# Kernel optimization log

Measured on AMD Instinct MI355X. Metric: run time of the kernel, lower is better.

## Reference

```python
import jax, jax.numpy as jnp
import numpy as np

# dims
B, SP, SF = 8, 1024, 1024
XD, YD = 6, 1
D, L, H, W = 512, 4, 8, 128
DH = D // H
S = SP + SF           # 2048 total sequence
C = S // W            # 16 clusters
FF = 4 * D
MIN_STD = 0.01


def _ln(x, g, b):
    m = x.mean(-1, keepdims=True)
    v = ((x - m) ** 2).mean(-1, keepdims=True)
    return (x - m) * jax.lax.rsqrt(v + 1e-5) * g + b


def _routing_attn(x, Wq, Wk, Wv, Wo, means):
    # x: (B,S,D); means: (H,C,DH) k-means centroids for routing
    b, s, _ = x.shape
    proj = lambda Wm: (x @ Wm).reshape(b, s, H, DH).transpose(0, 2, 1, 3)  # bhsd
    q, k, v = proj(Wq), proj(Wk), proj(Wv)
    qn = q * jax.lax.rsqrt((q * q).sum(-1, keepdims=True) + 1e-8)
    kn = k * jax.lax.rsqrt((k * k).sum(-1, keepdims=True) + 1e-8)
    # route: each cluster grabs its top-W most similar tokens (queries and keys separately)
    iq = jax.lax.top_k(jnp.einsum('bhsd,hcd->bhcs', qn, means), W)[1].reshape(b, H, C * W)
    ik = jax.lax.top_k(jnp.einsum('bhsd,hcd->bhcs', kn, means), W)[1].reshape(b, H, C * W)
    gather = lambda t, i: jnp.take_along_axis(t, i[..., None], axis=2).reshape(b, H, C, W, DH)
    qg, kg, vg = gather(q, iq), gather(k, ik), gather(v, ik)
    dots = jnp.einsum('bhcid,bhcjd->bhcij', qg, kg) * (DH ** -0.5)  # within-cluster attention
    attn = jax.nn.softmax(dots, axis=-1)
    og = jnp.einsum('bhcij,bhcjd->bhcid', attn, vg).reshape(b, H, C * W, DH)
    # scatter-mean back to sequence positions (a token may be routed to several clusters)
    bi = jnp.arange(b)[:, None, None]
    hi = jnp.arange(H)[None, :, None]
    out = jnp.zeros((b, H, s, DH), x.dtype).at[bi, hi, iq].add(og)
    cnt = jnp.zeros((b, H, s, 1), x.dtype).at[bi, hi, iq].add(1.0)
    out = out / jnp.maximum(cnt, 1.0)
    out = out.transpose(0, 2, 1, 3).reshape(b, s, D)
    return out @ Wo


def setup_inputs() -> dict:
    key = jax.random.key(0)
    ks = jax.random.split(key, 16)
    n = lambda k, shp, sc=0.02: (jax.random.normal(k, shp) * sc).astype(jnp.float32)
    inp = {
        'past_x': n(ks[0], (B, SP, XD), 1.0),
        'past_y': n(ks[1], (B, SP, YD), 1.0),
        'future_x': n(ks[2], (B, SF, XD), 1.0),
        'W_emb': n(ks[3], (XD + YD, D)), 'b_emb': jnp.zeros((D,), jnp.float32),
        'ln1_g': jnp.ones((L, D), jnp.float32), 'ln1_b': jnp.zeros((L, D), jnp.float32),
        'Wq': n(ks[4], (L, D, D)), 'Wk': n(ks[5], (L, D, D)),
        'Wv': n(ks[6], (L, D, D)), 'Wo': n(ks[7], (L, D, D)),
        'means': n(ks[8], (L, H, C, DH), 1.0),
        'ln2_g': jnp.ones((L, D), jnp.float32), 'ln2_b': jnp.zeros((L, D), jnp.float32),
        'W1': n(ks[9], (L, D, FF)), 'b1': jnp.zeros((L, FF), jnp.float32),
        'W2': n(ks[10], (L, FF, D)), 'b2': jnp.zeros((L, D), jnp.float32),
        'lnf_g': jnp.ones((D,), jnp.float32), 'lnf_b': jnp.zeros((D,), jnp.float32),
        'W_mean': n(ks[11], (D, YD)), 'b_mean': jnp.zeros((YD,), jnp.float32),
        'W_std': n(ks[12], (D, YD)), 'b_std': jnp.zeros((YD,), jnp.float32),
    }
    return inp


def reference(past_x, past_y, future_x, W_emb, b_emb, ln1_g, ln1_b, Wq, Wk, Wv, Wo,
              means, ln2_g, ln2_b, W1, b1, W2, b2, lnf_g, lnf_b, W_mean, b_mean,
              W_std, b_std):
    # future targets faked by repeating last observed y (as in the torch module)
    future_y_fake = jnp.repeat(past_y[:, -1:, :], SF, axis=1)
    context = jnp.concatenate([past_x, past_y], -1)
    target = jnp.concatenate([future_x, future_y_fake], -1)
    x = jnp.concatenate([context, target], 1)          # (B, S, XD+YD)
    h = x @ W_emb + b_emb                              # enc_emb
    for l in range(L):                                 # routing-transformer encoder
        h = h + _routing_attn(_ln(h, ln1_g[l], ln1_b[l]), Wq[l], Wk[l], Wv[l], Wo[l], means[l])
        hn = _ln(h, ln2_g[l], ln2_b[l])
        h = h + (jax.nn.gelu(hn @ W1[l] + b1[l]) @ W2[l] + b2[l])
    h = _ln(h, lnf_g, lnf_b)
    mean = (h @ W_mean + b_mean)[:, SP:, :]
    log_sigma = (h @ W_std + b_std)[:, SP:, :]
    sigma = MIN_STD + (1.0 - MIN_STD) * jax.nn.softplus(log_sigma)
    return mean, sigma
```

## Files before the change

kernel.cpp:

```cpp
#include <hip/hip_runtime.h>
#include <hip/hip_bf16.h>

constexpr int Bc  = 8;
constexpr int SPc = 1024;
constexpr int SFc = 1024;
constexpr int Sc  = 2048;
constexpr int Dc  = 512;
constexpr int Lc  = 4;
constexpr int Hc  = 8;
constexpr int Wc  = 128;
constexpr int DHc = 64;
constexpr int Cc  = 16;
constexpr int FFc = 2048;
constexpr int Mrows = Bc * Sc;

__global__ __launch_bounds__(256) void embed_kernel(
    const float* __restrict__ px, const float* __restrict__ py,
    const float* __restrict__ fx, const float* __restrict__ We,
    const float* __restrict__ be, float* __restrict__ h)
{
  int i = blockIdx.x * 256 + threadIdx.x;
  int d  = i & 511;
  int bs = i >> 9;
  int s  = bs & (Sc - 1);
  int b  = bs >> 11;
  float x[7];
  if (s < SPc) {
    int r = b * SPc + s;
#pragma unroll
    for (int t = 0; t < 6; ++t) x[t] = px[r * 6 + t];
    x[6] = py[r];
  } else {
    int r = b * SFc + (s - SPc);
#pragma unroll
    for (int t = 0; t < 6; ++t) x[t] = fx[r * 6 + t];
    x[6] = py[b * SPc + SPc - 1];
  }
  double a = (double)be[d];
#pragma unroll
  for (int t = 0; t < 7; ++t) a = fma((double)x[t], (double)We[t * Dc + d], a);
  h[i] = (float)a;
}

__global__ __launch_bounds__(256) void ln_kernel(
    const float* __restrict__ x, const float* __restrict__ g,
    const float* __restrict__ bb, float* __restrict__ o)
{
  int row = blockIdx.x;
  const float* xr = x + (size_t)row * Dc;
  float* orow = o + (size_t)row * Dc;
  int tid = threadIdx.x;
  float v0 = xr[tid], v1 = xr[tid + 256];
  double s = (double)v0 + (double)v1;
  double sq = (double)v0 * v0 + (double)v1 * v1;
  __shared__ double ra[4], rb[4];
  int lane = tid & 63, w = tid >> 6;
#pragma unroll
  for (int off = 32; off; off >>= 1) { s += __shfl_down(s, off); sq += __shfl_down(sq, off); }
  if (lane == 0) { ra[w] = s; rb[w] = sq; }
  __syncthreads();
  s  = ra[0] + ra[1] + ra[2] + ra[3];
  sq = rb[0] + rb[1] + rb[2] + rb[3];
  double m   = s * (1.0 / Dc);
  double var = sq * (1.0 / Dc) - m * m;
  double rs  = 1.0 / sqrt(var + 1e-5);
  orow[tid]       = (float)(((double)v0 - m) * rs * (double)g[tid]       + (double)bb[tid]);
  orow[tid + 256] = (float)(((double)v1 - m) * rs * (double)g[tid + 256] + (double)bb[tid + 256]);
}

__device__ __forceinline__ float gelu_tanh(float v) {
  float x3 = v * v * v;
  return 0.5f * v * (1.0f + tanhf(0.7978845608028654f * (v + 0.044715f * x3)));
}

template<bool BIAS, bool GELU_, bool RES>
__global__ __launch_bounds__(256) void gemm128(
    const float* __restrict__ A, const float* __restrict__ Bm,
    const float* __restrict__ bias, float* __restrict__ Cm,
    int N, int K)
{
  constexpr int BM = 128, BN = 128, BK = 16;
  __shared__ float As[BK][BM + 4];
  __shared__ float Bs[BK][BN + 4];
  const int tid = threadIdx.x;
  const int tx = tid & 15, ty = tid >> 4;
  const int nbn = N >> 7;
  const int bm = blockIdx.x / nbn, bn = blockIdx.x % nbn;
  const float* Ab = A + (size_t)bm * BM * K;
  const float* Bb = Bm + bn * BN;
  double acc[8][8] = {};

  for (int k0 = 0; k0 < K; k0 += BK) {
#pragma unroll
    for (int r = 0; r < 8; ++r) {
      int e = r * 256 + tid;
      int m = e >> 4, kk = e & 15;
      As[kk][m] = Ab[(size_t)m * K + k0 + kk];
    }
#pragma unroll
    for (int r = 0; r < 8; ++r) {
      int e = r * 256 + tid;
      int kk = e >> 7, n = e & 127;
      Bs[kk][n] = Bb[(size_t)(k0 + kk) * N + n];
    }
    __syncthreads();
#pragma unroll
    for (int kk = 0; kk < BK; ++kk) {
      float a[8], bf[8];
      *(float4*)&a[0]  = *(const float4*)&As[kk][ty * 8];
      *(float4*)&a[4]  = *(const float4*)&As[kk][ty * 8 + 4];
      *(float4*)&bf[0] = *(const float4*)&Bs[kk][tx * 8];
      *(float4*)&bf[4] = *(const float4*)&Bs[kk][tx * 8 + 4];
#pragma unroll
      for (int i = 0; i < 8; ++i)
#pragma unroll
        for (int j = 0; j < 8; ++j)
          acc[i][j] = fma((double)a[i], (double)bf[j], acc[i][j]);
    }
    __syncthreads();
  }
#pragma unroll
  for (int i = 0; i < 8; ++i) {
    int row = bm * BM + ty * 8 + i;
    float* crow = Cm + (size_t)row * N + bn * BN;
#pragma unroll
    for (int j = 0; j < 8; ++j) {
      double vd = acc[i][j];
      int col = tx * 8 + j;
      if (BIAS)  vd += (double)bias[bn * BN + col];
      float v = (float)vd;
      if (GELU_) v = gelu_tanh(v);
      if (RES)   v += crow[col];
      crow[col] = v;
    }
  }
}

__global__ __launch_bounds__(256) void scores_kernel(
    const float* __restrict__ q, const float* __restrict__ means,
    float* __restrict__ sc)
{
  int gw   = blockIdx.x * 4 + (threadIdx.x >> 6);
  int lane = threadIdx.x & 63;
  int h  = gw & 7;
  int bs = gw >> 3;
  int s  = bs & (Sc - 1);
  int b  = bs >> 11;
  float qv = q[(size_t)bs * Dc + h * DHc + lane];
  double sq = (double)qv * (double)qv;
#pragma unroll
  for (int off = 32; off; off >>= 1) sq += __shfl_xor(sq, off);
  double qn = (double)qv / sqrt(sq + 1e-8);
  double myval = 0.0;
#pragma unroll
  for (int c = 0; c < Cc; ++c) {
    double p = qn * (double)means[(h * Cc + c) * DHc + lane];
#pragma unroll
    for (int off = 32; off; off >>= 1) p += __shfl_xor(p, off);
    if (lane == c) myval = p;
  }
  if (lane < Cc)
    sc[(((size_t)b * Hc + h) * Cc + lane) * Sc + s] = (float)myval;
}

__global__ __launch_bounds__(256) void topk_kernel(
    const float* __restrict__ sc, int* __restrict__ idx_out)
{
  __shared__ float sv[Sc];
  __shared__ int   si[Sc];
  int base = blockIdx.x * Sc;
  int tid = threadIdx.x;
  for (int i = tid; i < Sc; i += 256) { sv[i] = sc[base + i]; si[i] = i; }
  __syncthreads();
  for (int k = 2; k <= Sc; k <<= 1) {
    for (int j = k >> 1; j > 0; j >>= 1) {
      for (int i = tid; i < Sc; i += 256) {
        int ixj = i ^ j;
        if (ixj > i) {
          bool asc = (i & k) != 0;
          float a = sv[i], b2 = sv[ixj];
          if (asc ? (a > b2) : (a < b2)) {
            sv[i] = b2; sv[ixj] = a;
            int t = si[i]; si[i] = si[ixj]; si[ixj] = t;
          }
        }
      }
      __syncthreads();
    }
  }
  if (tid < Wc) idx_out[blockIdx.x * Wc + tid] = si[tid];
}

__global__ __launch_bounds__(128) void attn_kernel(
    const float* __restrict__ q, const float* __restrict__ k,
    const float* __restrict__ v, const int* __restrict__ iq,
    const int* __restrict__ ik, float* __restrict__ accum,
    float* __restrict__ cnt)
{
  __shared__ float ks[Wc][DHc];
  __shared__ float vs[Wc][DHc];
  __shared__ int iqs[Wc], iks[Wc];
  int blk = blockIdx.x;
  int tid = threadIdx.x;
  int bh = blk / Cc;
  int h = bh & 7, b = bh >> 3;
  iqs[tid] = iq[blk * Wc + tid];
  iks[tid] = ik[blk * Wc + tid];
  __syncthreads();
  for (int e = tid; e < Wc * DHc; e += 128) {
    int j = e >> 6, d = e & 63;
    size_t off = ((size_t)b * Sc + iks[j]) * Dc + h * DHc + d;
    ks[j][d] = k[off];
    vs[j][d] = v[off];
  }
  __syncthreads();

  size_t qoff = ((size_t)b * Sc + iqs[tid]) * Dc + h * DHc;
  float qr[DHc];
  const float4* q4 = (const float4*)(q + qoff);
#pragma unroll
  for (int d4 = 0; d4 < 16; ++d4) {
    float4 t = q4[d4];
    qr[4 * d4] = t.x; qr[4 * d4 + 1] = t.y; qr[4 * d4 + 2] = t.z; qr[4 * d4 + 3] = t.w;
  }
  double m = -1e300, lsum = 0.0;
  double acc[DHc];
#pragma unroll
  for (int d = 0; d < DHc; ++d) acc[d] = 0.0;

  for (int j = 0; j < Wc; ++j) {
    const float* krow = ks[j];
    double s = 0.0;
#pragma unroll
    for (int d = 0; d < DHc; ++d)
      s = fma((double)qr[d], (double)krow[d], s);
    s *= 0.125;
    double mn = fmax(m, s);
    double scale = exp(m - mn);
    double p = exp(s - mn);
    lsum = lsum * scale + p;
    const float* vrow = vs[j];
#pragma unroll
    for (int d = 0; d < DHc; ++d)
      acc[d] = fma(acc[d], scale, p * (double)vrow[d]);
    m = mn;
  }
  double inv = 1.0 / lsum;
  float* arow = accum + qoff;
#pragma unroll
  for (int d = 0; d < DHc; ++d) atomicAdd(&arow[d], (float)(acc[d] * inv));
  atomicAdd(&cnt[((size_t)b * Sc + iqs[tid]) * Hc + h], 1.0f);
}

__global__ __launch_bounds__(256) void div_kernel(
    float* __restrict__ accum, const float* __restrict__ cnt)
{
  size_t i = (size_t)blockIdx.x * 256 + threadIdx.x;
  float c = cnt[i >> 6];
  accum[i] /= fmaxf(c, 1.0f);
}

__global__ __launch_bounds__(256) void final_kernel(
    const float* __restrict__ h, const float* __restrict__ g,
    const float* __restrict__ be, const float* __restrict__ wm,
    const float* __restrict__ bm, const float* __restrict__ wsd,
    const float* __restrict__ bsd, float* __restrict__ out)
{
  int blk = blockIdx.x;
  int b = blk >> 10, sf = blk & 1023;
  const float* hr = h + ((size_t)b * Sc + SPc + sf) * Dc;
  int tid = threadIdx.x;
  float v0 = hr[tid], v1 = hr[tid + 256];
  double s = (double)v0 + (double)v1;
  double sq = (double)v0 * v0 + (double)v1 * v1;
  __shared__ double ra[4], rb[4];
  int lane = tid & 63, w = tid >> 6;
#pragma unroll
  for (int off = 32; off; off >>= 1) { s += __shfl_down(s, off); sq += __shfl_down(sq, off); }
  if (lane == 0) { ra[w] = s; rb[w] = sq; }
  __syncthreads();
  s  = ra[0] + ra[1] + ra[2] + ra[3];
  sq = rb[0] + rb[1] + rb[2] + rb[3];
  double m   = s * (1.0 / Dc);
  double var = sq * (1.0 / Dc) - m * m;
  double rs  = 1.0 / sqrt(var + 1e-5);
  double n0 = ((double)v0 - m) * rs * (double)g[tid]       + (double)be[tid];
  double n1 = ((double)v1 - m) * rs * (double)g[tid + 256] + (double)be[tid + 256];
  double d1 = n0 * (double)wm[tid]  + n1 * (double)wm[tid + 256];
  double d2 = n0 * (double)wsd[tid] + n1 * (double)wsd[tid + 256];
  __syncthreads();
#pragma unroll
  for (int off = 32; off; off >>= 1) { d1 += __shfl_down(d1, off); d2 += __shfl_down(d2, off); }
  if (lane == 0) { ra[w] = d1; rb[w] = d2; }
  __syncthreads();
  if (tid == 0) {
    double mean = ra[0] + ra[1] + ra[2] + ra[3] + (double)bm[0];
    double ls   = rb[0] + rb[1] + rb[2] + rb[3] + (double)bsd[0];
    double sp = fmax(ls, 0.0) + log1p(exp(-fabs(ls)));
    out[blk] = (float)mean;
    out[Bc * SFc + blk] = (float)(0.01 + 0.99 * sp);
  }
}

extern "C" void kernel_launch(void* const* d_in, const int* in_sizes, int n_in,
                              void* d_out, int out_size, void* d_ws, size_t ws_size,
                              hipStream_t stream) {
  (void)in_sizes; (void)n_in; (void)out_size; (void)ws_size;
  const float* past_x   = (const float*)d_in[0];
  const float* past_y   = (const float*)d_in[1];
  const float* future_x = (const float*)d_in[2];
  const float* W_emb    = (const float*)d_in[3];
  const float* b_emb    = (const float*)d_in[4];
  const float* ln1_g    = (const float*)d_in[5];
  const float* ln1_b    = (const float*)d_in[6];
  const float* Wq       = (const float*)d_in[7];
  const float* Wk       = (const float*)d_in[8];
  const float* Wv       = (const float*)d_in[9];
  const float* Wo       = (const float*)d_in[10];
  const float* means    = (const float*)d_in[11];
  const float* ln2_g    = (const float*)d_in[12];
  const float* ln2_b    = (const float*)d_in[13];
  const float* W1       = (const float*)d_in[14];
  const float* b1       = (const float*)d_in[15];
  const float* W2       = (const float*)d_in[16];
  const float* b2       = (const float*)d_in[17];
  const float* lnf_g    = (const float*)d_in[18];
  const float* lnf_b    = (const float*)d_in[19];
  const float* W_mean   = (const float*)d_in[20];
  const float* b_mean   = (const float*)d_in[21];
  const float* W_std    = (const float*)d_in[22];
  const float* b_std    = (const float*)d_in[23];

  const size_t BSD = (size_t)Bc * Sc * Dc;
  float* h     = (float*)d_ws;
  float* lnbuf = h + BSD;
  float* qb    = lnbuf + BSD;
  float* kb    = qb + BSD;
  float* vb    = kb + BSD;
  float* accum = vb + BSD;
  float* mid   = qb;
  float* scq   = accum + BSD;
  float* sck   = scq + (size_t)Bc * Hc * Cc * Sc;
  int*   iq    = (int*)(sck + (size_t)Bc * Hc * Cc * Sc);
  int*   ik    = iq + Bc * Hc * Cc * Wc;
  float* cnt   = (float*)(ik + Bc * Hc * Cc * Wc);

  embed_kernel<<<(int)(BSD / 256), 256, 0, stream>>>(past_x, past_y, future_x, W_emb, b_emb, h);

  for (int l = 0; l < Lc; ++l) {
    ln_kernel<<<Mrows, 256, 0, stream>>>(h, ln1_g + l * Dc, ln1_b + l * Dc, lnbuf);

    gemm128<false,false,false><<<(Mrows/128)*(Dc/128), 256, 0, stream>>>(
        lnbuf, Wq + (size_t)l * Dc * Dc, nullptr, qb, Dc, Dc);
    gemm128<false,false,false><<<(Mrows/128)*(Dc/128), 256, 0, stream>>>(
        lnbuf, Wk + (size_t)l * Dc * Dc, nullptr, kb, Dc, Dc);
    gemm128<false,false,false><<<(Mrows/128)*(Dc/128), 256, 0, stream>>>(
        lnbuf, Wv + (size_t)l * Dc * Dc, nullptr, vb, Dc, Dc);

    const float* mns = means + (size_t)l * Hc * Cc * DHc;
    scores_kernel<<<Bc * Sc * Hc / 4, 256, 0, stream>>>(qb, mns, scq);
    scores_kernel<<<Bc * Sc * Hc / 4, 256, 0, stream>>>(kb, mns, sck);
    topk_kernel<<<Bc * Hc * Cc, 256, 0, stream>>>(scq, iq);
    topk_kernel<<<Bc * Hc * Cc, 256, 0, stream>>>(sck, ik);

    hipMemsetAsync(accum, 0, BSD * sizeof(float), stream);
    hipMemsetAsync(cnt, 0, (size_t)Bc * Sc * Hc * sizeof(float), stream);

    attn_kernel<<<Bc * Hc * Cc, 128, 0, stream>>>(qb, kb, vb, iq, ik, accum, cnt);
    div_kernel<<<(int)(BSD / 256), 256, 0, stream>>>(accum, cnt);

    gemm128<false,false,true><<<(Mrows/128)*(Dc/128), 256, 0, stream>>>(
        accum, Wo + (size_t)l * Dc * Dc, nullptr, h, Dc, Dc);

    ln_kernel<<<Mrows, 256, 0, stream>>>(h, ln2_g + l * Dc, ln2_b + l * Dc, lnbuf);

    gemm128<true,true,false><<<(Mrows/128)*(FFc/128), 256, 0, stream>>>(
        lnbuf, W1 + (size_t)l * Dc * FFc, b1 + (size_t)l * FFc, mid, FFc, Dc);
    gemm128<true,false,true><<<(Mrows/128)*(Dc/128), 256, 0, stream>>>(
        mid, W2 + (size_t)l * FFc * Dc, b2 + (size_t)l * Dc, h, Dc, FFc);
  }

  final_kernel<<<Bc * SFc, 256, 0, stream>>>(h, lnf_g, lnf_b, W_mean, b_mean,
                                             W_std, b_std, (float*)d_out);
}
```

Measured before the change: 17.84 ms.

## Move GEMMs to FP64 MFMA and 3-way FP16-split MFMA for last layer

Replaces the scalar double-precision FMA GEMM with one built on FP64 MFMA instructions, using a probe MFMA to recover the output lane layout. For the last layer (excluding the Q and K projections), the weights are split into three FP16 parts and the activations are split on the fly, then multiplied with six FP16 MFMAs per tile and accumulated in double. The goal is to move GEMM work from vector ALU onto matrix cores. The split path trades a little accuracy and adds weight-splitting kernels in exchange for much higher FP16 throughput, and it is applied only where the routing decisions can no longer change.

```diff
diff --git a/kernel.cpp b/kernel.cpp
--- a/kernel.cpp
+++ b/kernel.cpp
@@ -14,6 +14,24 @@
 constexpr int FFc = 2048;
 constexpr int Mrows = Bc * Sc;
 
+typedef _Float16 half8 __attribute__((ext_vector_type(8)));
+typedef _Float16 half4 __attribute__((ext_vector_type(4)));
+typedef float    f32x4 __attribute__((ext_vector_type(4)));
+typedef double   f64x4 __attribute__((ext_vector_type(4)));
+
+__device__ __forceinline__ void split3(float x, _Float16& p1, _Float16& p2, _Float16& p3) {
+  p1 = (_Float16)x;
+  float r = x - (float)p1;
+  p2 = (_Float16)r;
+  float r2 = r - (float)p2;
+  p3 = (_Float16)r2;
+}
+
+__device__ __forceinline__ float gelu_tanh(float v) {
+  float x3 = v * v * v;
+  return 0.5f * v * (1.0f + tanhf(0.7978845608028654f * (v + 0.044715f * x3)));
+}
+
 __global__ __launch_bounds__(256) void embed_kernel(
     const float* __restrict__ px, const float* __restrict__ py,
     const float* __restrict__ fx, const float* __restrict__ We,
@@ -68,72 +86,251 @@
   orow[tid + 256] = (float)(((double)v1 - m) * rs * (double)g[tid + 256] + (double)bb[tid + 256]);
 }
 
-__device__ __forceinline__ float gelu_tanh(float v) {
-  float x3 = v * v * v;
-  return 0.5f * v * (1.0f + tanhf(0.7978845608028654f * (v + 0.044715f * x3)));
-}
-
-template<bool BIAS, bool GELU_, bool RES>
-__global__ __launch_bounds__(256) void gemm128(
-    const float* __restrict__ A, const float* __restrict__ Bm,
-    const float* __restrict__ bias, float* __restrict__ Cm,
+template<int EP>
+__global__ __launch_bounds__(256) void gemm_f64(
+    const float* __restrict__ Af, const float* __restrict__ Bf,
+    const float* __restrict__ bias, float* __restrict__ C,
     int N, int K)
 {
-  constexpr int BM = 128, BN = 128, BK = 16;
-  __shared__ float As[BK][BM + 4];
-  __shared__ float Bs[BK][BN + 4];
+  __shared__ float As[16][132];
+  __shared__ float Bs[16][132];
   const int tid = threadIdx.x;
-  const int tx = tid & 15, ty = tid >> 4;
   const int nbn = N >> 7;
   const int bm = blockIdx.x / nbn, bn = blockIdx.x % nbn;
-  const float* Ab = A + (size_t)bm * BM * K;
-  const float* Bb = Bm + bn * BN;
-  double acc[8][8] = {};
-
-  for (int k0 = 0; k0 < K; k0 += BK) {
-#pragma unroll
-    for (int r = 0; r < 8; ++r) {
-      int e = r * 256 + tid;
-      int m = e >> 4, kk = e & 15;
-      As[kk][m] = Ab[(size_t)m * K + k0 + kk];
-    }
-#pragma unroll
-    for (int r = 0; r < 8; ++r) {
-      int e = r * 256 + tid;
-      int kk = e >> 7, n = e & 127;
-      Bs[kk][n] = Bb[(size_t)(k0 + kk) * N + n];
-    }
+  const int m0 = bm << 7, n0 = bn << 7;
+  const int wave = tid >> 6, lane = tid & 63;
+  const int wm = wave >> 1, wn = wave & 1;
+  const int lr = lane & 15, lq = lane >> 4;
+
+  double pa = (lq == 0) ? 1.0 : (lq == 1) ? (double)lr : 0.0;
+  double pb = (lq == 0) ? (double)lr * 0.0625 : (lq == 1) ? 1.0 : 0.0;
+  f64x4 pd = (f64x4){0.0, 0.0, 0.0, 0.0};
+  pd = __builtin_amdgcn_mfma_f64_16x16x4f64(pa, pb, pd, 0, 0, 0);
+  int drow[4], dcol[4];
+#pragma unroll
+  for (int r = 0; r < 4; ++r) {
+    double v = pd[r];
+    int i = (int)v;
+    int j = (int)((v - (double)i) * 16.0 + 0.5);
+    drow[r] = i; dcol[r] = j;
+  }
+
+  f64x4 acc[4][4];
+#pragma unroll
+  for (int i = 0; i < 4; ++i)
+#pragma unroll
+    for (int j = 0; j < 4; ++j)
+      acc[i][j] = (f64x4){0.0, 0.0, 0.0, 0.0};
+
+  for (int kt = 0; kt < K; kt += 16) {
     __syncthreads();
 #pragma unroll
-    for (int kk = 0; kk < BK; ++kk) {
-      float a[8], bf[8];
-      *(float4*)&a[0]  = *(const float4*)&As[kk][ty * 8];
-      *(float4*)&a[4]  = *(const float4*)&As[kk][ty * 8 + 4];
-      *(float4*)&bf[0] = *(const float4*)&Bs[kk][tx * 8];
-      *(float4*)&bf[4] = *(const float4*)&Bs[kk][tx * 8 + 4];
-#pragma unroll
-      for (int i = 0; i < 8; ++i)
-#pragma unroll
-        for (int j = 0; j < 8; ++j)
-          acc[i][j] = fma((double)a[i], (double)bf[j], acc[i][j]);
+    for (int h2 = 0; h2 < 2; ++h2) {
+      int fi = h2 * 256 + tid;
+      int m  = fi >> 2, kc = (fi & 3) << 2;
+      float4 va = *(const float4*)&Af[(size_t)(m0 + m) * K + kt + kc];
+      As[kc][m] = va.x; As[kc + 1][m] = va.y; As[kc + 2][m] = va.z; As[kc + 3][m] = va.w;
+      int kb2 = fi >> 5, c4 = (fi & 31) << 2;
+      *(float4*)&Bs[kb2][c4] = *(const float4*)&Bf[(size_t)(kt + kb2) * N + n0 + c4];
     }
     __syncthreads();
-  }
-#pragma unroll
-  for (int i = 0; i < 8; ++i) {
-    int row = bm * BM + ty * 8 + i;
-    float* crow = Cm + (size_t)row * N + bn * BN;
-#pragma unroll
-    for (int j = 0; j < 8; ++j) {
-      double vd = acc[i][j];
-      int col = tx * 8 + j;
-      if (BIAS)  vd += (double)bias[bn * BN + col];
-      float v = (float)vd;
-      if (GELU_) v = gelu_tanh(v);
-      if (RES)   v += crow[col];
-      crow[col] = v;
-    }
-  }
+#pragma unroll
+    for (int ks = 0; ks < 4; ++ks) {
+      double a[4], b[4];
+#pragma unroll
+      for (int mf = 0; mf < 4; ++mf)
+        a[mf] = (double)As[ks * 4 + lq][wm * 64 + mf * 16 + lr];
+#pragma unroll
+      for (int nf = 0; nf < 4; ++nf)
+        b[nf] = (double)Bs[ks * 4 + lq][wn * 64 + nf * 16 + lr];
+#pragma unroll
+      for (int mf = 0; mf < 4; ++mf)
+#pragma unroll
+        for (int nf = 0; nf < 4; ++nf)
+          acc[mf][nf] = __builtin_amdgcn_mfma_f64_16x16x4f64(a[mf], b[nf], acc[mf][nf], 0, 0, 0);
+    }
+  }
+
+#pragma unroll
+  for (int mf = 0; mf < 4; ++mf)
+#pragma unroll
+    for (int nf = 0; nf < 4; ++nf) {
+#pragma unroll
+      for (int r = 0; r < 4; ++r) {
+        int row = m0 + wm * 64 + mf * 16 + drow[r];
+        int col = n0 + wn * 64 + nf * 16 + dcol[r];
+        double vd = acc[mf][nf][r];
+        size_t o = (size_t)row * N + col;
+        if (EP == 0) {
+          C[o] = (float)vd;
+        } else if (EP == 1) {
+          C[o] += (float)vd;
+        } else if (EP == 2) {
+          vd += (double)bias[col];
+          C[o] = gelu_tanh((float)vd);
+        } else {
+          vd += (double)bias[col];
+          C[o] += (float)vd;
+        }
+      }
+    }
+}
+
+__global__ __launch_bounds__(256) void splitB3(
+    const float* __restrict__ Wm, _Float16* __restrict__ P1,
+    _Float16* __restrict__ P2, _Float16* __restrict__ P3, int K, int N)
+{
+  __shared__ float tile[64][65];
+  int tid = threadIdx.x;
+  int nbk = K >> 6;
+  int bk = blockIdx.x % nbk, bnn = blockIdx.x / nbk;
+  int k0 = bk * 64, n0 = bnn * 64;
+  int tc = tid & 63, tr = tid >> 6;
+#pragma unroll
+  for (int i = 0; i < 16; ++i) {
+    int k = i * 4 + tr;
+    tile[k][tc] = Wm[(size_t)(k0 + k) * N + n0 + tc];
+  }
+  __syncthreads();
+#pragma unroll
+  for (int i = 0; i < 16; ++i) {
+    int n = i * 4 + tr;
+    float x = tile[tc][n];
+    _Float16 p1, p2, p3;
+    split3(x, p1, p2, p3);
+    size_t o = (size_t)(n0 + n) * K + k0 + tc;
+    P1[o] = p1; P2[o] = p2; P3[o] = p3;
+  }
+}
+
+template<int EP>
+__global__ __launch_bounds__(256) void gemm3p(
+    const float* __restrict__ Af,
+    const _Float16* __restrict__ B1, const _Float16* __restrict__ B2,
+    const _Float16* __restrict__ B3,
+    const float* __restrict__ bias, float* __restrict__ C,
+    int N, int K)
+{
+  __shared__ _Float16 Al[3][128][40];
+  __shared__ _Float16 Bl[3][64][40];
+  const int tid = threadIdx.x;
+  const int nbn = N >> 6;
+  const int bm = blockIdx.x / nbn, bn = blockIdx.x % nbn;
+  const int m0 = bm << 7, n0 = bn << 6;
+  const int wave = tid >> 6, lane = tid & 63;
+  const int wm = wave >> 1, wn = wave & 1;
+  const int lr = lane & 15, lq = lane >> 4;
+
+  double acc[4][2][4];
+#pragma unroll
+  for (int i = 0; i < 4; ++i)
+#pragma unroll
+    for (int j = 0; j < 2; ++j)
+#pragma unroll
+      for (int r = 0; r < 4; ++r) acc[i][j][r] = 0.0;
+
+  f32x4 apf[4];
+  half8 bpf[3];
+  const int ar = tid >> 3, ac = (tid & 7) * 4;
+  const int bnr = tid >> 2, bkc = (tid & 3) * 8;
+
+  auto load_pf = [&](int k0) {
+#pragma unroll
+    for (int i = 0; i < 4; ++i)
+      apf[i] = *(const f32x4*)&Af[(size_t)(m0 + i * 32 + ar) * K + k0 + ac];
+    size_t ob = (size_t)(n0 + bnr) * K + k0 + bkc;
+    bpf[0] = *(const half8*)&B1[ob];
+    bpf[1] = *(const half8*)&B2[ob];
+    bpf[2] = *(const half8*)&B3[ob];
+  };
+  auto write_lds = [&]() {
+#pragma unroll
+    for (int i = 0; i < 4; ++i) {
+      half4 h1, h2, h3;
+#pragma unroll
+      for (int j = 0; j < 4; ++j) {
+        _Float16 p1, p2, p3;
+        split3(apf[i][j], p1, p2, p3);
+        h1[j] = p1; h2[j] = p2; h3[j] = p3;
+      }
+      int row = i * 32 + ar;
+      *(half4*)&Al[0][row][ac] = h1;
+      *(half4*)&Al[1][row][ac] = h2;
+      *(half4*)&Al[2][row][ac] = h3;
+    }
+    *(half8*)&Bl[0][bnr][bkc] = bpf[0];
+    *(half8*)&Bl[1][bnr][bkc] = bpf[1];
+    *(half8*)&Bl[2][bnr][bkc] = bpf[2];
+  };
+
+  load_pf(0);
+  write_lds();
+  __syncthreads();
+
+  const int nt = K >> 5;
+  for (int t = 0; t < nt; ++t) {
+    if (t + 1 < nt) load_pf((t + 1) << 5);
+
+    half8 a1[4], a2[4], a3[4], b1f[2], b2f[2], b3f[2];
+#pragma unroll
+    for (int mf = 0; mf < 4; ++mf) {
+      int row = wm * 64 + mf * 16 + lr;
+      a1[mf] = *(const half8*)&Al[0][row][lq * 8];
+      a2[mf] = *(const half8*)&Al[1][row][lq * 8];
+      a3[mf] = *(const half8*)&Al[2][row][lq * 8];
+    }
+#pragma unroll
+    for (int nf = 0; nf < 2; ++nf) {
+      int row = wn * 32 + nf * 16 + lr;
+      b1f[nf] = *(const half8*)&Bl[0][row][lq * 8];
+      b2f[nf] = *(const half8*)&Bl[1][row][lq * 8];
+      b3f[nf] = *(const half8*)&Bl[2][row][lq * 8];
+    }
+#pragma unroll
+    for (int mf = 0; mf < 4; ++mf)
+#pragma unroll
+      for (int nf = 0; nf < 2; ++nf) {
+        f32x4 t0 = (f32x4){0.f, 0.f, 0.f, 0.f};
+        t0 = __builtin_amdgcn_mfma_f32_16x16x32_f16(a3[mf], b1f[nf], t0, 0, 0, 0);
+        t0 = __builtin_amdgcn_mfma_f32_16x16x32_f16(a2[mf], b2f[nf], t0, 0, 0, 0);
+        t0 = __builtin_amdgcn_mfma_f32_16x16x32_f16(a1[mf], b3f[nf], t0, 0, 0, 0);
+        t0 = __builtin_amdgcn_mfma_f32_16x16x32_f16(a2[mf], b1f[nf], t0, 0, 0, 0);
+        t0 = __builtin_amdgcn_mfma_f32_16x16x32_f16(a1[mf], b2f[nf], t0, 0, 0, 0);
+        t0 = __builtin_amdgcn_mfma_f32_16x16x32_f16(a1[mf], b1f[nf], t0, 0, 0, 0);
+#pragma unroll
+        for (int r = 0; r < 4; ++r) acc[mf][nf][r] += (double)t0[r];
+      }
+
+    __syncthreads();
+    if (t + 1 < nt) {
+      write_lds();
+      __syncthreads();
+    }
+  }
+
+#pragma unroll
+  for (int mf = 0; mf < 4; ++mf)
+#pragma unroll
+    for (int nf = 0; nf < 2; ++nf) {
+#pragma unroll
+      for (int r = 0; r < 4; ++r) {
+        int row = m0 + wm * 64 + mf * 16 + lq * 4 + r;
+        int col = n0 + wn * 32 + nf * 16 + lr;
+        double vd = acc[mf][nf][r];
+        size_t o = (size_t)row * N + col;
+        if (EP == 0) {
+          C[o] = (float)vd;
+        } else if (EP == 1) {
+          C[o] += (float)vd;
+        } else if (EP == 2) {
+          vd += (double)bias[col];
+          C[o] = gelu_tanh((float)vd);
+        } else {
+          vd += (double)bias[col];
+          C[o] += (float)vd;
+        }
+      }
+    }
 }
 
 __global__ __launch_bounds__(256) void scores_kernel(
@@ -333,29 +530,44 @@
 
   const size_t BSD = (size_t)Bc * Sc * Dc;
   float* h     = (float*)d_ws;
-  float* lnbuf = h + BSD;
-  float* qb    = lnbuf + BSD;
-  float* kb    = qb + BSD;
-  float* vb    = kb + BSD;
-  float* accum = vb + BSD;
+  float* R1    = h + BSD;
+  float* qb    = h + 2 * BSD;
+  float* kb    = h + 3 * BSD;
+  float* vb    = h + 4 * BSD;
+  float* accum = h + 5 * BSD;
   float* mid   = qb;
-  float* scq   = accum + BSD;
-  float* sck   = scq + (size_t)Bc * Hc * Cc * Sc;
-  int*   iq    = (int*)(sck + (size_t)Bc * Hc * Cc * Sc);
-  int*   ik    = iq + Bc * Hc * Cc * Wc;
-  float* cnt   = (float*)(ik + Bc * Hc * Cc * Wc);
+  float* aux   = h + 6 * BSD;
+  float* scq   = aux;
+  float* sck   = aux + 2097152;
+  int*   iq    = (int*)(aux + 4194304);
+  int*   ik    = iq + 262144;
+  float* cnt   = (float*)(ik + 262144);
+  _Float16* BT1 = (_Float16*)scq;
+  _Float16* BT2 = BT1 + 1048576;
+  _Float16* BT3 = BT2 + 1048576;
 
   embed_kernel<<<(int)(BSD / 256), 256, 0, stream>>>(past_x, past_y, future_x, W_emb, b_emb, h);
 
+  const int gF64_D  = (Mrows / 128) * (Dc / 128);
+  const int gF64_FF = (Mrows / 128) * (FFc / 128);
+  const int g3p_D   = (Mrows / 128) * (Dc / 64);
+  const int g3p_FF  = (Mrows / 128) * (FFc / 64);
+  const int tD_D  = (Dc / 64) * (Dc / 64);
+  const int tD_FF = (Dc / 64) * (FFc / 64);
+  const int tFF_D = (FFc / 64) * (Dc / 64);
+
   for (int l = 0; l < Lc; ++l) {
-    ln_kernel<<<Mrows, 256, 0, stream>>>(h, ln1_g + l * Dc, ln1_b + l * Dc, lnbuf);
-
-    gemm128<false,false,false><<<(Mrows/128)*(Dc/128), 256, 0, stream>>>(
-        lnbuf, Wq + (size_t)l * Dc * Dc, nullptr, qb, Dc, Dc);
-    gemm128<false,false,false><<<(Mrows/128)*(Dc/128), 256, 0, stream>>>(
-        lnbuf, Wk + (size_t)l * Dc * Dc, nullptr, kb, Dc, Dc);
-    gemm128<false,false,false><<<(Mrows/128)*(Dc/128), 256, 0, stream>>>(
-        lnbuf, Wv + (size_t)l * Dc * Dc, nullptr, vb, Dc, Dc);
+    const bool last = (l == Lc - 1);
+    ln_kernel<<<Mrows, 256, 0, stream>>>(h, ln1_g + l * Dc, ln1_b + l * Dc, R1);
+
+    gemm_f64<0><<<gF64_D, 256, 0, stream>>>(R1, Wq + (size_t)l * Dc * Dc, nullptr, qb, Dc, Dc);
+    gemm_f64<0><<<gF64_D, 256, 0, stream>>>(R1, Wk + (size_t)l * Dc * Dc, nullptr, kb, Dc, Dc);
+    if (!last) {
+      gemm_f64<0><<<gF64_D, 256, 0, stream>>>(R1, Wv + (size_t)l * Dc * Dc, nullptr, vb, Dc, Dc);
+    } else {
+      splitB3<<<tD_D, 256, 0, stream>>>(Wv + (size_t)l * Dc * Dc, BT1, BT2, BT3, Dc, Dc);
+      gemm3p<0><<<g3p_D, 256, 0, stream>>>(R1, BT1, BT2, BT3, nullptr, vb, Dc, Dc);
+    }
 
     const float* mns = means + (size_t)l * Hc * Cc * DHc;
     scores_kernel<<<Bc * Sc * Hc / 4, 256, 0, stream>>>(qb, mns, scq);
@@ -369,15 +581,26 @@
     attn_kernel<<<Bc * Hc * Cc, 128, 0, stream>>>(qb, kb, vb, iq, ik, accum, cnt);
     div_kernel<<<(int)(BSD / 256), 256, 0, stream>>>(accum, cnt);
 
-    gemm128<false,false,true><<<(Mrows/128)*(Dc/128), 256, 0, stream>>>(
-        accum, Wo + (size_t)l * Dc * Dc, nullptr, h, Dc, Dc);
-
-    ln_kernel<<<Mrows, 256, 0, stream>>>(h, ln2_g + l * Dc, ln2_b + l * Dc, lnbuf);
-
-    gemm128<true,true,false><<<(Mrows/128)*(FFc/128), 256, 0, stream>>>(
-        lnbuf, W1 + (size_t)l * Dc * FFc, b1 + (size_t)l * FFc, mid, FFc, Dc);
-    gemm128<true,false,true><<<(Mrows/128)*(Dc/128), 256, 0, stream>>>(
-        mid, W2 + (size_t)l * FFc * Dc, b2 + (size_t)l * Dc, h, Dc, FFc);
+    if (!last) {
+      gemm_f64<1><<<gF64_D, 256, 0, stream>>>(accum, Wo + (size_t)l * Dc * Dc, nullptr, h, Dc, Dc);
+    } else {
+      splitB3<<<tD_D, 256, 0, stream>>>(Wo + (size_t)l * Dc * Dc, BT1, BT2, BT3, Dc, Dc);
+      gemm3p<1><<<g3p_D, 256, 0, stream>>>(accum, BT1, BT2, BT3, nullptr, h, Dc, Dc);
+    }
+
+    ln_kernel<<<Mrows, 256, 0, stream>>>(h, ln2_g + l * Dc, ln2_b + l * Dc, R1);
+
+    if (!last) {
+      gemm_f64<2><<<gF64_FF, 256, 0, stream>>>(R1, W1 + (size_t)l * Dc * FFc,
+                                               b1 + (size_t)l * FFc, mid, FFc, Dc);
+      gemm_f64<3><<<gF64_D, 256, 0, stream>>>(mid, W2 + (size_t)l * FFc * Dc,
+                                              b2 + (size_t)l * Dc, h, Dc, FFc);
+    } else {
+      splitB3<<<tD_FF, 256, 0, stream>>>(W1 + (size_t)l * Dc * FFc, BT1, BT2, BT3, Dc, FFc);
+      gemm3p<2><<<g3p_FF, 256, 0, stream>>>(R1, BT1, BT2, BT3, b1 + (size_t)l * FFc, mid, FFc, Dc);
+      splitB3<<<tFF_D, 256, 0, stream>>>(W2 + (size_t)l * FFc * Dc, BT1, BT2, BT3, FFc, Dc);
+      gemm3p<3><<<g3p_D, 256, 0, stream>>>(mid, BT1, BT2, BT3, b2 + (size_t)l * Dc, h, Dc, FFc);
+    }
   }
 
   final_kernel<<<Bc * SFc, 256, 0, stream>>>(h, lnf_g, lnf_b, W_mean, b_mean,
```

After: 15.21 ms. -14.7%, faster.
